# Optimization experiments

Measured on AMD Instinct MI355X. Metric: run time of the kernel, lower is better.

## Reference

```python
import jax, jax.numpy as jnp
import numpy as np

N = 50000      # nodes
E = 600000     # edges
DIN = 128
H1, H2, H3 = 128, 128, 64
EPS = 1e-5


def setup_inputs() -> dict:
    key = jax.random.key(0)
    ks = jax.random.split(key, 12)
    x = jax.random.normal(ks[0], (N, DIN), jnp.float32)
    edge_index = jax.random.randint(ks[1], (2, E), 0, N, dtype=jnp.int32).astype(jnp.int64)
    s = lambda f: np.float32(1.0 / np.sqrt(f))
    W1 = jax.random.normal(ks[2], (DIN, H1), jnp.float32) * s(DIN)
    b1 = jnp.zeros((H1,), jnp.float32)
    W2 = jax.random.normal(ks[3], (H1, H2), jnp.float32) * s(H1)
    b2 = jnp.zeros((H2,), jnp.float32)
    W3 = jax.random.normal(ks[4], (H2, H3), jnp.float32) * s(H2)
    b3 = jnp.zeros((H3,), jnp.float32)
    g1 = 1.0 + 0.1 * jax.random.normal(ks[5], (H1,), jnp.float32)
    be1 = 0.1 * jax.random.normal(ks[6], (H1,), jnp.float32)
    g2 = 1.0 + 0.1 * jax.random.normal(ks[7], (H2,), jnp.float32)
    be2 = 0.1 * jax.random.normal(ks[8], (H2,), jnp.float32)
    return {"x": x, "edge_index": edge_index, "W1": W1, "b1": b1, "g1": g1,
            "be1": be1, "W2": W2, "b2": b2, "g2": g2, "be2": be2,
            "W3": W3, "b3": b3}


def _gcn(h_in, W, b, src_sl, dst_sl, norm, n):
    # GCNConv: h = X W; out_i = sum_{j->i} norm_ij * h_j + b  (self-loops included)
    h = h_in @ W
    msg = h[src_sl] * norm[:, None]          # [E+N, F] gather + scale
    out = jax.ops.segment_sum(msg, dst_sl, num_segments=n)
    return out + b


def _bn(x, g, b):
    # training-mode BatchNorm1d over nodes (biased variance, eps=1e-5)
    m = x.mean(0)
    v = x.var(0)
    return g * (x - m) * jax.lax.rsqrt(v + EPS) + b


def reference(x, edge_index, W1, b1, g1, be1, W2, b2, g2, be2, W3, b3):
    src, dst = edge_index[0], edge_index[1]
    loops = jnp.arange(N, dtype=src.dtype)
    src_sl = jnp.concatenate([src, loops])
    dst_sl = jnp.concatenate([dst, loops])
    deg = jax.ops.segment_sum(jnp.ones_like(dst_sl, jnp.float32), dst_sl,
                              num_segments=N)
    dinv = jnp.where(deg > 0, jax.lax.rsqrt(deg), 0.0)
    norm = dinv[src_sl] * dinv[dst_sl]       # symmetric D^-1/2 (A+I) D^-1/2

    h = _gcn(x, W1, b1, src_sl, dst_sl, norm, N)
    h = jax.nn.relu(_bn(h, g1, be1))         # dropout is identity in eval mode
    h = _gcn(h, W2, b2, src_sl, dst_sl, norm, N)
    h = jax.nn.relu(_bn(h, g2, be2))
    out = _gcn(h, W3, b3, src_sl, dst_sl, norm, N)  # [N, 64]
    return out
```

## Files before the change

### kernel.cpp

```cpp
#include <hip/hip_runtime.h>
#include <hip/hip_bf16.h>


typedef __attribute__((ext_vector_type(8))) short short8;
typedef __attribute__((ext_vector_type(4))) float f32x4;

__device__ inline unsigned short f2bf(float f) {
    unsigned int u = __float_as_uint(f);
    return (unsigned short)((u + 0x7fff + ((u >> 16) & 1)) >> 16);
}
__device__ inline float bf2f_lo(unsigned int p) { return __uint_as_float(p << 16); }
__device__ inline float bf2f_hi(unsigned int p) { return __uint_as_float(p & 0xffff0000u); }

__device__ inline void bf4_acc(uint2 v, float* a) {
    a[0] += bf2f_lo(v.x); a[1] += bf2f_hi(v.x);
    a[2] += bf2f_lo(v.y); a[3] += bf2f_hi(v.y);
}

__global__ void prep_kernel(const int* __restrict__ dst, int E,
                            int* __restrict__ deg,
                            const float* __restrict__ x,
                            unsigned short* __restrict__ xb, int total4,
                            const float* __restrict__ W1,
                            const float* __restrict__ W2,
                            const float* __restrict__ W3,
                            unsigned short* __restrict__ wt1,
                            unsigned short* __restrict__ wt2,
                            unsigned short* __restrict__ wt3,
                            int EB, int XB) {
    const int b = blockIdx.x;
    const int t = threadIdx.x;
    if (b < EB) {
        int e = b * 256 + t;
        if (e < E) atomicAdd(deg + dst[e], 1);
    } else if (b < EB + XB) {
        int i = (b - EB) * 256 + t;
        if (i < total4) {
            float4 v = reinterpret_cast<const float4*>(x)[i];
            uint2 p;
            p.x = f2bf(v.x) | ((unsigned)f2bf(v.y) << 16);
            p.y = f2bf(v.z) | ((unsigned)f2bf(v.w) << 16);
            reinterpret_cast<uint2*>(xb)[i] = p;
        }
    } else if (b < EB + XB + 64) {
        int idx = (b - EB - XB) * 256 + t;
        int k = idx >> 7, nn = idx & 127;
        wt1[nn * 128 + k] = f2bf(W1[idx]);
    } else if (b < EB + XB + 128) {
        int idx = (b - EB - XB - 64) * 256 + t;
        int k = idx >> 7, nn = idx & 127;
        wt2[nn * 128 + k] = f2bf(W2[idx]);
    } else {
        int idx = (b - EB - XB - 128) * 256 + t;
        int k = idx >> 6, nn = idx & 63;
        wt3[nn * 128 + k] = f2bf(W3[idx]);
    }
}

__global__ __launch_bounds__(256) void prescan_kernel(
    const int* __restrict__ deg, int n, int B, float* __restrict__ dinv,
    int* __restrict__ bh, int* __restrict__ rowptr, int* __restrict__ bsum) {
    __shared__ int lh[64];
    __shared__ int sh[256];
    const int t = threadIdx.x, b = blockIdx.x;
    if (t < 64) lh[t] = 0;
    __syncthreads();
    const int base = b * 2048 + t * 8;
    int v[8];
    int run = 0;
#pragma unroll
    for (int j = 0; j < 8; ++j) {
        int idx = base + j;
        int d = 0;
        if (idx < n) {
            d = deg[idx];
            dinv[idx] = rsqrtf((float)(d + 1));
            atomicAdd(&lh[min(d, 63)], 1);
        }
        run += d;
        v[j] = run;
    }
    sh[t] = run;
    __syncthreads();
#pragma unroll
    for (int off = 1; off < 256; off <<= 1) {
        int add = (t >= off) ? sh[t - off] : 0;
        __syncthreads();
        sh[t] += add;
        __syncthreads();
    }
    int prev = (t > 0) ? sh[t - 1] : 0;
#pragma unroll
    for (int j = 0; j < 8; ++j) {
        int idx = base + j;
        if (idx < n) rowptr[idx + 1] = v[j] + prev;
    }
    if (t == 255) bsum[b] = sh[255];
    if (b == 0 && t == 0) rowptr[0] = 0;
    if (t < 64) bh[t * B + b] = lh[t];
}

__global__ void midscan_kernel(int* __restrict__ bh, int totalbh,
                               int* __restrict__ bsum, int B) {
    __shared__ int sh[256];
    const int t = threadIdx.x;
    int base = 0;
    for (int start = 0; start < totalbh; start += 256) {
        int i = start + t;
        int v = (i < totalbh) ? bh[i] : 0;
        sh[t] = v;
        __syncthreads();
#pragma unroll
        for (int off = 1; off < 256; off <<= 1) {
            int add = (t >= off) ? sh[t - off] : 0;
            __syncthreads();
            sh[t] += add;
            __syncthreads();
        }
        int excl = (t > 0 ? sh[t - 1] : 0) + base;
        if (i < totalbh) bh[i] = excl;
        base += sh[255];
        __syncthreads();
    }
    int v = (t < B) ? bsum[t] : 0;
    sh[t] = v;
    __syncthreads();
#pragma unroll
    for (int off = 1; off < 64; off <<= 1) {
        int add = (t >= off && t < 64) ? sh[t - off] : 0;
        __syncthreads();
        if (t < 64) sh[t] += add;
        __syncthreads();
    }
    if (t < B) bsum[t] = sh[t];
}

__global__ void place_scanC_kernel(const int* __restrict__ deg, int n, int B,
                                   const int* __restrict__ bh,
                                   const int* __restrict__ bsum,
                                   int* __restrict__ perm,
                                   int* __restrict__ rowptr) {
    const int t = threadIdx.x;
    if ((int)blockIdx.x < B) {
        const int b = blockIdx.x;
        __shared__ int lbase[64];
        __shared__ int lcur[64];
        if (t < 64) {
            lbase[t] = bh[t * B + b];
            lcur[t] = 0;
        }
        __syncthreads();
        const int lim = min((b + 1) * 2048, n);
        for (int i = b * 2048 + t; i < lim; i += 256) {
            int d = min(deg[i], 63);
            int r = atomicAdd(&lcur[d], 1);
            perm[lbase[d] + r] = i;
        }
    } else {
        const int c = blockIdx.x - B;
        if (c == 0) return;
        const int off = bsum[c - 1];
        const int lim = min((c + 1) * 2048, n);
        for (int i = c * 2048 + t; i < lim; i += 256) rowptr[i + 1] += off;
    }
}

__global__ void csr_build_kernel(const int* __restrict__ src,
                                 const int* __restrict__ dst, int E,
                                 int* __restrict__ rowptr,
                                 int* __restrict__ csr_src) {
    int e = blockIdx.x * blockDim.x + threadIdx.x;
    if (e < E) {
        int pos = atomicAdd(rowptr + dst[e], 1);
        csr_src[pos] = src[e];
    }
}

template <int NC, bool BN>
__global__ __launch_bounds__(256) void gemm_mfma(
    const unsigned short* __restrict__ A, const unsigned short* __restrict__ Wt,
    unsigned short* __restrict__ C, int n, const float* __restrict__ stats,
    const float* __restrict__ g, const float* __restrict__ be, float invn,
    const float* __restrict__ dinv) {
    __shared__ unsigned short Asd[64][136];
    __shared__ unsigned short Bsd[64][136];
    __shared__ float ssl[256];
    const int tid = threadIdx.x;
    const int wave = tid >> 6;
    const int lane = tid & 63;
    const int row0 = blockIdx.x * 64;
    const int col0 = blockIdx.y * 64;

    if (BN) {
        if (tid < 128) {
            float mean = stats[tid] * invn;
            float var = fmaf(-mean, mean, stats[128 + tid] * invn);
            float sc = g[tid] * rsqrtf(var + 1e-5f);
            ssl[tid] = sc;
            ssl[128 + tid] = fmaf(-mean, sc, be[tid]);
        }
        __syncthreads();
    }

    for (int idx = tid; idx < 64 * 16; idx += 256) {
        int r = idx >> 4;
        int c = (idx & 15) * 8;
        uint4 v = *reinterpret_cast<const uint4*>(Wt + (size_t)(col0 + r) * 128 + c);
        *reinterpret_cast<uint4*>(&Bsd[r][c]) = v;
    }
    for (int idx = tid; idx < 64 * 16; idx += 256) {
        int r = idx >> 4;
        int c = (idx & 15) * 8;
        int grow = row0 + r;
        uint4 v = make_uint4(0u, 0u, 0u, 0u);
        if (grow < n)
            v = *reinterpret_cast<const uint4*>(A + (size_t)grow * 128 + c);
        if (BN) {
            unsigned int p[4] = {v.x, v.y, v.z, v.w};
#pragma unroll
            for (int h = 0; h < 4; ++h) {
                int f = c + h * 2;
                float lo = fmaxf(fmaf(bf2f_lo(p[h]), ssl[f], ssl[128 + f]), 0.f);
                float hi = fmaxf(fmaf(bf2f_hi(p[h]), ssl[f + 1], ssl[129 + f]), 0.f);
                p[h] = f2bf(lo) | ((unsigned)f2bf(hi) << 16);
            }
            v = make_uint4(p[0], p[1], p[2], p[3]);
        }
        *reinterpret_cast<uint4*>(&Asd[r][c]) = v;
    }
    __syncthreads();

    f32x4 acc[4];
#pragma unroll
    for (int t = 0; t < 4; ++t) acc[t] = (f32x4)(0.f);

    const int l15 = lane & 15;
    const int quad = lane >> 4;
#pragma unroll
    for (int kb = 0; kb < 128; kb += 32) {
        short8 a = *reinterpret_cast<const short8*>(&Asd[wave * 16 + l15][kb + quad * 8]);
#pragma unroll
        for (int t = 0; t < 4; ++t) {
            short8 b = *reinterpret_cast<const short8*>(&Bsd[t * 16 + l15][kb + quad * 8]);
            acc[t] = __builtin_amdgcn_mfma_f32_16x16x32_bf16(a, b, acc[t], 0, 0, 0);
        }
    }

    const int rbase = row0 + wave * 16 + quad * 4;
    float dv[4] = {0.f, 0.f, 0.f, 0.f};
    if (rbase < n) {
        float4 d4 = *reinterpret_cast<const float4*>(dinv + rbase);
        dv[0] = d4.x; dv[1] = d4.y; dv[2] = d4.z; dv[3] = d4.w;
    }
#pragma unroll
    for (int t = 0; t < 4; ++t) {
        int col = col0 + t * 16 + l15;
#pragma unroll
        for (int r = 0; r < 4; ++r) {
            int row = rbase + r;
            if (row < n)
                C[(size_t)row * NC + col] = f2bf(acc[t][r] * dv[r]);
        }
    }
}

template <int F, bool STATS, bool OBF>
__global__ __launch_bounds__(256) void aggregate_kernel(
    const unsigned short* __restrict__ hs, const int* __restrict__ csr_src,
    const int* __restrict__ rowptr, const int* __restrict__ perm,
    const float* __restrict__ dinv, const float* __restrict__ bias,
    void* __restrict__ outp, int n, float* __restrict__ stats) {
    const int LANES = F / 4;
    const int GROUPS = 256 / LANES;
    const int lane = threadIdx.x % LANES;
    const int grp = threadIdx.x / LANES;
    const int fq = lane * 4;
    const float4 b4 = *reinterpret_cast<const float4*>(bias + fq);
    float s[4] = {}, sq[4] = {};

    const int stride = gridDim.x * GROUPS * 4;

    for (int j0 = (blockIdx.x * GROUPS + grp) * 4; j0 < n; j0 += stride) {
        const int nv = min(4, n - j0);
        int nd[4], e[4], end[4];
        float acc[4][4] = {};
#pragma unroll
        for (int q = 0; q < 4; ++q) {
            if (q < nv) {
                int node = perm[j0 + q];
                nd[q] = node;
                e[q] = (node == 0) ? 0 : rowptr[node - 1];
                end[q] = rowptr[node];
            } else {
                nd[q] = -1; e[q] = 0; end[q] = 0;
            }
        }
#pragma unroll
        for (int q = 0; q < 4; ++q)
            if (nd[q] >= 0)
                bf4_acc(*reinterpret_cast<const uint2*>(hs + (size_t)nd[q] * F + fq), acc[q]);
        int rem = end[0] - e[0];
#pragma unroll
        for (int q = 1; q < 4; ++q)
            if (q < nv) rem = min(rem, end[q] - e[q]);
        for (; rem >= 2; rem -= 2) {
            int i0[4], i1[4];
#pragma unroll
            for (int q = 0; q < 4; ++q) {
                i0[q] = csr_src[e[q]];
                i1[q] = csr_src[e[q] + 1];
                e[q] += 2;
            }
            uint2 v0[4], v1[4];
#pragma unroll
            for (int q = 0; q < 4; ++q) {
                v0[q] = *reinterpret_cast<const uint2*>(hs + (size_t)i0[q] * F + fq);
                v1[q] = *reinterpret_cast<const uint2*>(hs + (size_t)i1[q] * F + fq);
            }
#pragma unroll
            for (int q = 0; q < 4; ++q) {
                bf4_acc(v0[q], acc[q]);
                bf4_acc(v1[q], acc[q]);
            }
        }
#pragma unroll
        for (int q = 0; q < 4; ++q) {
            for (; e[q] < end[q]; ++e[q]) {
                int s0 = csr_src[e[q]];
                bf4_acc(*reinterpret_cast<const uint2*>(hs + (size_t)s0 * F + fq), acc[q]);
            }
        }
#pragma unroll
        for (int q = 0; q < 4; ++q) {
            if (nd[q] < 0) continue;
            const float di = dinv[nd[q]];
            float y[4];
            y[0] = fmaf(di, acc[q][0], b4.x);
            y[1] = fmaf(di, acc[q][1], b4.y);
            y[2] = fmaf(di, acc[q][2], b4.z);
            y[3] = fmaf(di, acc[q][3], b4.w);
            if (OBF) {
                uint2 p;
                p.x = f2bf(y[0]) | ((unsigned)f2bf(y[1]) << 16);
                p.y = f2bf(y[2]) | ((unsigned)f2bf(y[3]) << 16);
                *reinterpret_cast<uint2*>((unsigned short*)outp + (size_t)nd[q] * F + fq) = p;
            } else {
                *reinterpret_cast<float4*>((float*)outp + (size_t)nd[q] * F + fq) =
                    make_float4(y[0], y[1], y[2], y[3]);
            }
            if (STATS) {
#pragma unroll
                for (int j = 0; j < 4; ++j) {
                    s[j] += y[j];
                    sq[j] = fmaf(y[j], y[j], sq[j]);
                }
            }
        }
    }

    if (STATS) {
        __shared__ float sred[32][8];
#pragma unroll
        for (int q = 0; q < 8; ++q) {
            float v = (q < 4) ? s[q] : sq[q - 4];
            sred[lane][grp] = v;
            __syncthreads();
            if (grp == 0) {
                float t = 0.f;
#pragma unroll
                for (int g = 0; g < 8; ++g) t += sred[lane][g];
                int f = fq + (q & 3);
                atomicAdd(stats + ((q < 4) ? f : 128 + f), t);
            }
            __syncthreads();
        }
    }
}

extern "C" void kernel_launch(void* const* d_in, const int* in_sizes, int n_in,
                              void* d_out, int out_size, void* d_ws,
                              size_t ws_size, hipStream_t stream) {
    const float* x   = (const float*)d_in[0];
    const int*   ei  = (const int*)d_in[1];
    const float* W1  = (const float*)d_in[2];
    const float* b1  = (const float*)d_in[3];
    const float* g1  = (const float*)d_in[4];
    const float* be1 = (const float*)d_in[5];
    const float* W2  = (const float*)d_in[6];
    const float* b2  = (const float*)d_in[7];
    const float* g2  = (const float*)d_in[8];
    const float* be2 = (const float*)d_in[9];
    const float* W3  = (const float*)d_in[10];
    const float* b3  = (const float*)d_in[11];
    float* out = (float*)d_out;

    const int n = in_sizes[0] / 128;
    const int E = in_sizes[1] / 2;
    const int* src = ei;
    const int* dst = ei + E;

    const int B = (n + 2047) / 2048;

    float* wsf    = (float*)d_ws;
    float* stats1 = wsf;
    float* stats2 = stats1 + 256;
    int*   deg    = (int*)(stats2 + 256);
    float* dinv   = (float*)(deg + n);
    int*   bh     = (int*)(dinv + n + 64);
    int*   bsum   = bh + 64 * 32;
    int*   rowptr = bsum + 64;
    int*   perm   = rowptr + (n + 1);
    int*   csrsrc = perm + n;
    unsigned short* wt1 = (unsigned short*)(csrsrc + E);
    unsigned short* wt2 = wt1 + 128 * 128;
    unsigned short* wt3 = wt2 + 128 * 128;
    unsigned short* abuf = wt3 + 64 * 128;
    unsigned short* hsb  = abuf + (size_t)n * 128;

    const int EB = (E + 255) / 256;
    const int total4 = n * 32;
    const int XB = (total4 + 255) / 256;

    hipMemsetAsync(wsf, 0, (size_t)(512 + n) * 4, stream);
    prep_kernel<<<EB + XB + 160, 256, 0, stream>>>(dst, E, deg, x, abuf, total4,
                                                   W1, W2, W3, wt1, wt2, wt3,
                                                   EB, XB);
    prescan_kernel<<<B, 256, 0, stream>>>(deg, n, B, dinv, bh, rowptr, bsum);
    midscan_kernel<<<1, 256, 0, stream>>>(bh, 64 * B, bsum, B);
    place_scanC_kernel<<<2 * B, 256, 0, stream>>>(deg, n, B, bh, bsum, perm, rowptr);
    csr_build_kernel<<<EB, 256, 0, stream>>>(src, dst, E, rowptr, csrsrc);

    const int gemmRows = (n + 63) / 64;
    dim3 gemmGrid128(gemmRows, 2);
    dim3 gemmGrid64(gemmRows, 1);
    const int aggGrid = 512;
    const float invn = 1.0f / n;

    gemm_mfma<128, false><<<gemmGrid128, 256, 0, stream>>>(abuf, wt1, hsb, n, nullptr, nullptr, nullptr, invn, dinv);
    aggregate_kernel<128, true, true><<<aggGrid, 256, 0, stream>>>(hsb, csrsrc, rowptr, perm, dinv, b1, abuf, n, stats1);
    gemm_mfma<128, true><<<gemmGrid128, 256, 0, stream>>>(abuf, wt2, hsb, n, stats1, g1, be1, invn, dinv);
    aggregate_kernel<128, true, true><<<aggGrid, 256, 0, stream>>>(hsb, csrsrc, rowptr, perm, dinv, b2, abuf, n, stats2);
    gemm_mfma<64, true><<<gemmGrid64, 256, 0, stream>>>(abuf, wt3, hsb, n, stats2, g2, be2, invn, dinv);
    aggregate_kernel<64, false, false><<<aggGrid, 256, 0, stream>>>(hsb, csrsrc, rowptr, perm, dinv, b3, out, n, nullptr);
}
```

Before: 426.0 us.

## Bucket CSR neighbor lists by source range to improve gather locality

Splits each destination node's CSR row into 8 sub-buckets keyed by source-node range, so the neighbor lists are partially sorted by source index. The intent is better cache locality when the aggregate kernels gather feature rows, since neighbors processed at the same time come from nearby source regions. In exchange the count array grows to 8 entries per node, which adds memset, scan and atomic work in the CSR build stage. The degree histogram now uses global atomics.

```diff
diff --git a/kernel.cpp b/kernel.cpp
--- a/kernel.cpp
+++ b/kernel.cpp
@@ -17,8 +17,9 @@
     a[2] += bf2f_lo(v.y); a[3] += bf2f_hi(v.y);
 }
 
-__global__ void prep_kernel(const int* __restrict__ dst, int E,
-                            int* __restrict__ deg,
+__global__ void prep_kernel(const int* __restrict__ src,
+                            const int* __restrict__ dst, int E,
+                            int* __restrict__ cnt, float bscale,
                             const float* __restrict__ x,
                             unsigned short* __restrict__ xb, int total4,
                             const float* __restrict__ W1,
@@ -32,7 +33,11 @@
     const int t = threadIdx.x;
     if (b < EB) {
         int e = b * 256 + t;
-        if (e < E) atomicAdd(deg + dst[e], 1);
+        if (e < E) {
+            int s = src[e], d = dst[e];
+            int bk = min(7, (int)((float)s * bscale));
+            atomicAdd(cnt + d * 8 + bk, 1);
+        }
     } else if (b < EB + XB) {
         int i = (b - EB) * 256 + t;
         if (i < total4) {
@@ -58,27 +63,27 @@
 }
 
 __global__ __launch_bounds__(256) void prescan_kernel(
-    const int* __restrict__ deg, int n, int B, float* __restrict__ dinv,
-    int* __restrict__ bh, int* __restrict__ rowptr, int* __restrict__ bsum) {
-    __shared__ int lh[64];
+    const int* __restrict__ cnt, int n, int BH, float* __restrict__ dinv,
+    int* __restrict__ deg, int* __restrict__ bh, int* __restrict__ rowptr2,
+    int* __restrict__ bsum) {
     __shared__ int sh[256];
     const int t = threadIdx.x, b = blockIdx.x;
-    if (t < 64) lh[t] = 0;
-    __syncthreads();
-    const int base = b * 2048 + t * 8;
+    const int node = b * 256 + t;
+    const int base = node * 8;
+    const bool valid = node < n;
     int v[8];
     int run = 0;
 #pragma unroll
     for (int j = 0; j < 8; ++j) {
-        int idx = base + j;
-        int d = 0;
-        if (idx < n) {
-            d = deg[idx];
-            dinv[idx] = rsqrtf((float)(d + 1));
-            atomicAdd(&lh[min(d, 63)], 1);
-        }
-        run += d;
+        int c = valid ? cnt[base + j] : 0;
+        run += c;
         v[j] = run;
+    }
+    if (valid) {
+        dinv[node] = rsqrtf((float)(run + 1));
+        int db = min(run, 63);
+        deg[node] = db;
+        atomicAdd(bh + db * BH + (node >> 11), 1);
     }
     sh[t] = run;
     __syncthreads();
@@ -92,16 +97,14 @@
     int prev = (t > 0) ? sh[t - 1] : 0;
 #pragma unroll
     for (int j = 0; j < 8; ++j) {
-        int idx = base + j;
-        if (idx < n) rowptr[idx + 1] = v[j] + prev;
+        if (valid) rowptr2[base + j + 1] = v[j] + prev;
     }
     if (t == 255) bsum[b] = sh[255];
-    if (b == 0 && t == 0) rowptr[0] = 0;
-    if (t < 64) bh[t * B + b] = lh[t];
+    if (b == 0 && t == 0) rowptr2[0] = 0;
 }
 
 __global__ void midscan_kernel(int* __restrict__ bh, int totalbh,
-                               int* __restrict__ bsum, int B) {
+                               int* __restrict__ bsum, int B2) {
     __shared__ int sh[256];
     const int t = threadIdx.x;
     int base = 0;
@@ -122,57 +125,60 @@
         base += sh[255];
         __syncthreads();
     }
-    int v = (t < B) ? bsum[t] : 0;
+    int v = (t < B2) ? bsum[t] : 0;
     sh[t] = v;
     __syncthreads();
 #pragma unroll
-    for (int off = 1; off < 64; off <<= 1) {
-        int add = (t >= off && t < 64) ? sh[t - off] : 0;
-        __syncthreads();
-        if (t < 64) sh[t] += add;
-        __syncthreads();
-    }
-    if (t < B) bsum[t] = sh[t];
-}
-
-__global__ void place_scanC_kernel(const int* __restrict__ deg, int n, int B,
-                                   const int* __restrict__ bh,
+    for (int off = 1; off < 256; off <<= 1) {
+        int add = (t >= off) ? sh[t - off] : 0;
+        __syncthreads();
+        sh[t] += add;
+        __syncthreads();
+    }
+    if (t < B2) bsum[t] = sh[t];
+}
+
+__global__ void place_scanC_kernel(const int* __restrict__ deg, int n, int BH,
+                                   int B2, const int* __restrict__ bh,
                                    const int* __restrict__ bsum,
                                    int* __restrict__ perm,
-                                   int* __restrict__ rowptr) {
+                                   int* __restrict__ rowptr2) {
     const int t = threadIdx.x;
-    if ((int)blockIdx.x < B) {
+    if ((int)blockIdx.x < BH) {
         const int b = blockIdx.x;
         __shared__ int lbase[64];
         __shared__ int lcur[64];
         if (t < 64) {
-            lbase[t] = bh[t * B + b];
+            lbase[t] = bh[t * BH + b];
             lcur[t] = 0;
         }
         __syncthreads();
         const int lim = min((b + 1) * 2048, n);
         for (int i = b * 2048 + t; i < lim; i += 256) {
-            int d = min(deg[i], 63);
+            int d = deg[i];
             int r = atomicAdd(&lcur[d], 1);
             perm[lbase[d] + r] = i;
         }
     } else {
-        const int c = blockIdx.x - B;
+        const int c = blockIdx.x - BH;
         if (c == 0) return;
         const int off = bsum[c - 1];
-        const int lim = min((c + 1) * 2048, n);
-        for (int i = c * 2048 + t; i < lim; i += 256) rowptr[i + 1] += off;
+        const int total2 = n * 8;
+        const int lim = min((c + 1) * 2048, total2);
+        for (int i = c * 2048 + t; i < lim; i += 256) rowptr2[i + 1] += off;
     }
 }
 
 __global__ void csr_build_kernel(const int* __restrict__ src,
                                  const int* __restrict__ dst, int E,
-                                 int* __restrict__ rowptr,
-                                 int* __restrict__ csr_src) {
+                                 int* __restrict__ rowptr2,
+                                 int* __restrict__ csr_src, float bscale) {
     int e = blockIdx.x * blockDim.x + threadIdx.x;
     if (e < E) {
-        int pos = atomicAdd(rowptr + dst[e], 1);
-        csr_src[pos] = src[e];
+        int s = src[e], d = dst[e];
+        int bk = min(7, (int)((float)s * bscale));
+        int pos = atomicAdd(rowptr2 + d * 8 + bk, 1);
+        csr_src[pos] = s;
     }
 }
 
@@ -267,7 +273,7 @@
 template <int F, bool STATS, bool OBF>
 __global__ __launch_bounds__(256) void aggregate_kernel(
     const unsigned short* __restrict__ hs, const int* __restrict__ csr_src,
-    const int* __restrict__ rowptr, const int* __restrict__ perm,
+    const int* __restrict__ rowptr2, const int* __restrict__ perm,
     const float* __restrict__ dinv, const float* __restrict__ bias,
     void* __restrict__ outp, int n, float* __restrict__ stats) {
     const int LANES = F / 4;
@@ -289,8 +295,9 @@
             if (q < nv) {
                 int node = perm[j0 + q];
                 nd[q] = node;
-                e[q] = (node == 0) ? 0 : rowptr[node - 1];
-                end[q] = rowptr[node];
+                int k = node * 8;
+                e[q] = (node == 0) ? 0 : rowptr2[k - 1];
+                end[q] = rowptr2[k + 7];
             } else {
                 nd[q] = -1; e[q] = 0; end[q] = 0;
             }
@@ -399,17 +406,20 @@
     const int* src = ei;
     const int* dst = ei + E;
 
-    const int B = (n + 2047) / 2048;
+    const int BH = (n + 2047) / 2048;
+    const int B2 = (n + 255) / 256;
+    const float bscale = 8.0f / (float)n;
 
     float* wsf    = (float*)d_ws;
     float* stats1 = wsf;
     float* stats2 = stats1 + 256;
-    int*   deg    = (int*)(stats2 + 256);
+    int*   bh     = (int*)(stats2 + 256);
+    int*   cnt    = bh + 2048;
+    int*   deg    = cnt + (size_t)n * 8;
     float* dinv   = (float*)(deg + n);
-    int*   bh     = (int*)(dinv + n + 64);
-    int*   bsum   = bh + 64 * 32;
-    int*   rowptr = bsum + 64;
-    int*   perm   = rowptr + (n + 1);
+    int*   bsum   = (int*)(dinv + n + 64);
+    int*   rowptr2= bsum + 256;
+    int*   perm   = rowptr2 + (size_t)n * 8 + 1;
     int*   csrsrc = perm + n;
     unsigned short* wt1 = (unsigned short*)(csrsrc + E);
     unsigned short* wt2 = wt1 + 128 * 128;
@@ -421,14 +431,15 @@
     const int total4 = n * 32;
     const int XB = (total4 + 255) / 256;
 
-    hipMemsetAsync(wsf, 0, (size_t)(512 + n) * 4, stream);
-    prep_kernel<<<EB + XB + 160, 256, 0, stream>>>(dst, E, deg, x, abuf, total4,
+    hipMemsetAsync(wsf, 0, (size_t)(512 + 2048 + (size_t)n * 8) * 4, stream);
+    prep_kernel<<<EB + XB + 160, 256, 0, stream>>>(src, dst, E, cnt, bscale,
+                                                   x, abuf, total4,
                                                    W1, W2, W3, wt1, wt2, wt3,
                                                    EB, XB);
-    prescan_kernel<<<B, 256, 0, stream>>>(deg, n, B, dinv, bh, rowptr, bsum);
-    midscan_kernel<<<1, 256, 0, stream>>>(bh, 64 * B, bsum, B);
-    place_scanC_kernel<<<2 * B, 256, 0, stream>>>(deg, n, B, bh, bsum, perm, rowptr);
-    csr_build_kernel<<<EB, 256, 0, stream>>>(src, dst, E, rowptr, csrsrc);
+    prescan_kernel<<<B2, 256, 0, stream>>>(cnt, n, BH, dinv, deg, bh, rowptr2, bsum);
+    midscan_kernel<<<1, 256, 0, stream>>>(bh, 64 * BH, bsum, B2);
+    place_scanC_kernel<<<BH + B2, 256, 0, stream>>>(deg, n, BH, B2, bh, bsum, perm, rowptr2);
+    csr_build_kernel<<<EB, 256, 0, stream>>>(src, dst, E, rowptr2, csrsrc, bscale);
 
     const int gemmRows = (n + 63) / 64;
     dim3 gemmGrid128(gemmRows, 2);
@@ -437,9 +448,9 @@
     const float invn = 1.0f / n;
 
     gemm_mfma<128, false><<<gemmGrid128, 256, 0, stream>>>(abuf, wt1, hsb, n, nullptr, nullptr, nullptr, invn, dinv);
-    aggregate_kernel<128, true, true><<<aggGrid, 256, 0, stream>>>(hsb, csrsrc, rowptr, perm, dinv, b1, abuf, n, stats1);
+    aggregate_kernel<128, true, true><<<aggGrid, 256, 0, stream>>>(hsb, csrsrc, rowptr2, perm, dinv, b1, abuf, n, stats1);
     gemm_mfma<128, true><<<gemmGrid128, 256, 0, stream>>>(abuf, wt2, hsb, n, stats1, g1, be1, invn, dinv);
-    aggregate_kernel<128, true, true><<<aggGrid, 256, 0, stream>>>(hsb, csrsrc, rowptr, perm, dinv, b2, abuf, n, stats2);
+    aggregate_kernel<128, true, true><<<aggGrid, 256, 0, stream>>>(hsb, csrsrc, rowptr2, perm, dinv, b2, abuf, n, stats2);
     gemm_mfma<64, true><<<gemmGrid64, 256, 0, stream>>>(abuf, wt3, hsb, n, stats2, g2, be2, invn, dinv);
-    aggregate_kernel<64, false, false><<<aggGrid, 256, 0, stream>>>(hsb, csrsrc, rowptr, perm, dinv, b3, out, n, nullptr);
-}
+    aggregate_kernel<64, false, false><<<aggGrid, 256, 0, stream>>>(hsb, csrsrc, rowptr2, perm, dinv, b3, out, n, nullptr);
+}
```

Result: slower. 500.4 us (+17.5%).
